# Kernel tuning notes

Measured on AMD Instinct MI355X. Metric: run time of the kernel, lower is better.

The kernel has to match this reference:

```python
import jax, jax.numpy as jnp
import numpy as np

KS = 3      # kernel_size
PAD = 1     # padding
GROUPS = 4

def _patches(a, H, W):
    # a: [B, C, H+2*PAD, W+2*PAD] -> [B, C, H, W, KS, KS]
    return jnp.stack([
        jnp.stack([a[:, :, i:i + H, j:j + W] for j in range(KS)], axis=-1)
        for i in range(KS)], axis=-2)

def setup_inputs() -> dict:
    key = jax.random.key(0)
    ks = jax.random.split(key, 7)
    B, Cin, Cout, H, W = 8, 256, 256, 64, 64
    std = np.sqrt(2.0 / Cout)  # kaiming fan_out
    return {
        "x": jax.random.normal(ks[0], (B, Cin, H, W), jnp.float32),
        "y": jax.random.normal(ks[1], (B, Cin, H, W), jnp.float32),
        "wq": jax.random.normal(ks[2], (Cout, Cin), jnp.float32) * std,
        "wk": jax.random.normal(ks[3], (Cout, Cin), jnp.float32) * std,
        "wv": jax.random.normal(ks[4], (Cout, Cin), jnp.float32) * std,
        "rel_h": jax.random.normal(ks[5], (Cout // 2, 1, 1, KS, 1), jnp.float32),
        "rel_w": jax.random.normal(ks[6], (Cout // 2, 1, 1, 1, KS), jnp.float32),
    }

def reference(x, y, wq, wk, wv, rel_h, rel_w):
    B, _, H, W = x.shape
    Cout = wq.shape[0]
    half = Cout // 2
    xp = jnp.pad(x, ((0, 0), (0, 0), (PAD, PAD), (PAD, PAD)))
    q = jnp.einsum('oi,bihw->bohw', wq, y)          # [B,Cout,H,W]
    k = jnp.einsum('oi,bihw->bohw', wk, xp)         # [B,Cout,H+2,W+2]
    v = jnp.einsum('oi,bihw->bohw', wv, xp)
    kp = _patches(k, H, W)                          # [B,Cout,H,W,KS,KS]
    vp = _patches(v, H, W)
    kp = jnp.concatenate([kp[:, :half] + rel_h[None], kp[:, half:] + rel_w[None]], axis=1)
    cg = Cout // GROUPS
    kp = kp.reshape(B, GROUPS, cg, H, W, KS * KS)
    vp = vp.reshape(B, GROUPS, cg, H, W, KS * KS)
    qg = q.reshape(B, GROUPS, cg, H, W, 1)
    attn = jax.nn.softmax(qg * kp, axis=-1)         # per-channel softmax over window
    out = jnp.einsum('bnchwk,bnchwk->bnchw', attn, vp)
    return out.reshape(B, Cout, H, W)
```

## Files before the change

### kernel.cpp

```cpp
#include <hip/hip_runtime.h>
#include <hip/hip_bf16.h>
#include <stdint.h>

typedef __attribute__((ext_vector_type(8))) short short8;
typedef __attribute__((ext_vector_type(4))) float floatx4;
typedef __attribute__((ext_vector_type(4))) unsigned int uintx4;
typedef __attribute__((ext_vector_type(2))) unsigned int uintx2;
typedef unsigned int u32;

#define HH 64
#define WW 64
#define HWSZ 4096
#define BB 8
#define CIN 256
#define COUT 256
#define NTOT 32768

#define GLL16(g, l)                                                            \
    __builtin_amdgcn_global_load_lds(                                          \
        (const __attribute__((address_space(1))) u32*)(const void*)(g),        \
        (__attribute__((address_space(3))) u32*)(void*)(l), 16, 0, 0)

__device__ __forceinline__ unsigned short f2b(float f) {
    union { float f; unsigned int u; } v; v.f = f;
    unsigned int r = v.u + 0x7FFFu + ((v.u >> 16) & 1u);
    return (unsigned short)(r >> 16);
}
__device__ __forceinline__ float b2f(unsigned short h) {
    union { unsigned int u; float f; } v; v.u = ((unsigned int)h) << 16;
    return v.f;
}

__global__ __launch_bounds__(256) void transpose_cast(
        const float* __restrict__ y, const float* __restrict__ x,
        unsigned short* __restrict__ yT, unsigned short* __restrict__ xT) {
    __shared__ float lt[64 * 65];
    int zz = blockIdx.z;
    int which = zz & 1;
    int b = zz >> 1;
    const float* src = which ? x : y;
    unsigned short* dst = which ? xT : yT;
    int p0 = blockIdx.x * 64;
    int c0 = blockIdx.y * 64;
    int t = threadIdx.x;

    const float* sp = src + ((size_t)b * CIN + c0) * HWSZ + p0;
    int chL = t >> 4;
    int pxL = (t & 15) * 4;
    #pragma unroll
    for (int pass = 0; pass < 4; ++pass) {
        int ch = chL + pass * 16;
        float4 v = *(const float4*)(sp + (size_t)ch * HWSZ + pxL);
        lt[ch * 65 + pxL + 0] = v.x;
        lt[ch * 65 + pxL + 1] = v.y;
        lt[ch * 65 + pxL + 2] = v.z;
        lt[ch * 65 + pxL + 3] = v.w;
    }
    __syncthreads();

    int c8 = (t & 7) * 8;
    int pxR = t >> 3;
    unsigned short* dp = dst + ((size_t)b * HWSZ + p0) * CIN + c0 + c8;
    #pragma unroll
    for (int pass = 0; pass < 2; ++pass) {
        int px = pxR + pass * 32;
        unsigned int dw[4];
        #pragma unroll
        for (int j = 0; j < 4; ++j) {
            float lo = lt[(c8 + 2 * j) * 65 + px];
            float hi = lt[(c8 + 2 * j + 1) * 65 + px];
            dw[j] = (unsigned int)f2b(lo) | ((unsigned int)f2b(hi) << 16);
        }
        *(uintx4*)(dp + (size_t)px * CIN) = (uintx4){dw[0], dw[1], dw[2], dw[3]};
    }
}

__global__ void wcast(const float* __restrict__ wq, const float* __restrict__ wk,
                      const float* __restrict__ wv,
                      unsigned short* __restrict__ wqb, unsigned short* __restrict__ wkb,
                      unsigned short* __restrict__ wvb) {
    int idx = blockIdx.x * 256 + threadIdx.x;
    wqb[idx] = f2b(wq[idx]);
    wkb[idx] = f2b(wk[idx]);
    wvb[idx] = f2b(wv[idx]);
}

__global__ __launch_bounds__(256)
void gemm_qkv(const unsigned short* __restrict__ wqb, const unsigned short* __restrict__ wkb,
              const unsigned short* __restrict__ wvb,
              const unsigned short* __restrict__ yT, const unsigned short* __restrict__ xT,
              unsigned short* __restrict__ Qb, unsigned short* __restrict__ Kb,
              unsigned short* __restrict__ Vb) {
    __shared__ unsigned short lA[2][128 * 32];
    __shared__ unsigned short lB[2][128 * 32];

    int z = blockIdx.z;
    const unsigned short* Wb = (z == 0) ? wqb : (z == 1) ? wkb : wvb;
    const unsigned short* In = (z == 0) ? yT : xT;
    unsigned short* Out = (z == 0) ? Qb : (z == 1) ? Kb : Vb;

    int n0 = blockIdx.x * 128;
    int m0 = blockIdx.y * 128;
    int t = threadIdx.x;
    int lane = t & 63;
    int wave = t >> 6;
    int quad = lane >> 4;
    int l16 = lane & 15;
    int wm = (wave >> 1) * 64;
    int wn = (wave & 1) * 64;

    int sA0 = t >> 2;
    int cch = (t & 3) * 8;
    int sB0 = t >> 2;
    int sB1 = 64 + (t >> 2);
    int gnB0 = 4 * (sB0 & 31) + (sB0 >> 5);
    int gnB1 = 4 * (sB1 & 31) + (sB1 >> 5);

    const unsigned short* gA0 = Wb + (size_t)(m0 + sA0) * CIN + cch;
    const unsigned short* gA1 = Wb + (size_t)(m0 + sA0 + 64) * CIN + cch;
    const unsigned short* gB0 = In + (size_t)(n0 + gnB0) * CIN + cch;
    const unsigned short* gB1 = In + (size_t)(n0 + gnB1) * CIN + cch;

    floatx4 acc[4][4];
    #pragma unroll
    for (int mi = 0; mi < 4; ++mi)
        #pragma unroll
        for (int ni = 0; ni < 4; ++ni)
            acc[mi][ni] = (floatx4){0.f, 0.f, 0.f, 0.f};

    #pragma unroll
    for (int it = 0; it < 4; ++it) {
        int k0 = it * 64;
        #pragma unroll
        for (int bsel = 0; bsel < 2; ++bsel) {
            int ko = k0 + bsel * 32;
            unsigned short* dA = lA[bsel] + wave * 512;
            unsigned short* dB = lB[bsel] + wave * 512;
            GLL16(gA0 + ko, dA);
            GLL16(gA1 + ko, dA + 2048);
            GLL16(gB0 + ko, dB);
            GLL16(gB1 + ko, dB + 2048);
        }
        __syncthreads();

        #pragma unroll
        for (int bsel = 0; bsel < 2; ++bsel) {
            short8 af[4], bf[4];
            #pragma unroll
            for (int mi = 0; mi < 4; ++mi)
                af[mi] = *(const short8*)(lA[bsel] + (wm + mi * 16 + l16) * 32 + quad * 8);
            #pragma unroll
            for (int ni = 0; ni < 4; ++ni)
                bf[ni] = *(const short8*)(lB[bsel] + (ni * 32 + (wn >> 2) + l16) * 32 + quad * 8);
            #pragma unroll
            for (int mi = 0; mi < 4; ++mi)
                #pragma unroll
                for (int ni = 0; ni < 4; ++ni)
                    acc[mi][ni] = __builtin_amdgcn_mfma_f32_16x16x32_bf16(af[mi], bf[ni], acc[mi][ni], 0, 0, 0);
        }
        __syncthreads();
    }

    int colb = n0 + wn + 4 * l16;
    #pragma unroll
    for (int mi = 0; mi < 4; ++mi) {
        #pragma unroll
        for (int r = 0; r < 4; ++r) {
            int row = m0 + wm + mi * 16 + quad * 4 + r;
            unsigned int lo = (unsigned int)f2b(acc[mi][0][r]) | ((unsigned int)f2b(acc[mi][1][r]) << 16);
            unsigned int hi = (unsigned int)f2b(acc[mi][2][r]) | ((unsigned int)f2b(acc[mi][3][r]) << 16);
            *(uintx2*)(Out + (size_t)row * NTOT + colb) = (uintx2){lo, hi};
        }
    }
}

__global__ __launch_bounds__(256)
void attn(const unsigned short* __restrict__ Q,
          const unsigned short* __restrict__ K,
          const unsigned short* __restrict__ V,
          const float* __restrict__ rel_h,
          const float* __restrict__ rel_w,
          float* __restrict__ out) {
    int gid = blockIdx.x * 256 + threadIdx.x;
    int w8 = gid & 7;
    int w0 = w8 << 3;
    int h = (gid >> 3) & 63;
    int c = (gid >> 9) & 255;
    int b = gid >> 17;

    size_t nb = (size_t)c * NTOT + (size_t)b * HWSZ;
    const unsigned short* Kp = K + nb;
    const unsigned short* Vp = V + nb;

    short8 qr = *(const short8*)(Q + nb + h * 64 + w0);

    bool use_h = (c < 128);
    float rel3[3];
    if (use_h) {
        rel3[0] = rel_h[c * 3 + 0]; rel3[1] = rel_h[c * 3 + 1]; rel3[2] = rel_h[c * 3 + 2];
    } else {
        int cc = c - 128;
        rel3[0] = rel_w[cc * 3 + 0]; rel3[1] = rel_w[cc * 3 + 1]; rel3[2] = rel_w[cc * 3 + 2];
    }
    float rr[9];
    #pragma unroll
    for (int r = 0; r < 3; ++r)
        #pragma unroll
        for (int j = 0; j < 3; ++j)
            rr[r * 3 + j] = use_h ? rel3[r] : rel3[j];

    int e0 = (w0 > 0) ? w0 - 1 : 0;
    int e9 = (w0 < 56) ? w0 + 8 : 63;
    bool okL = (w0 > 0);
    bool okR = (w0 < 56);

    float kb[3][10], vb[3][10];
    #pragma unroll
    for (int r = 0; r < 3; ++r) {
        int ihr = h + r - 1;
        bool rok = (unsigned)ihr < 64u;
        int ihc = ihr < 0 ? 0 : (ihr > 63 ? 63 : ihr);
        int ro = ihc * 64;
        short8 km = *(const short8*)(Kp + ro + w0);
        short8 vm = *(const short8*)(Vp + ro + w0);
        float ke0 = b2f(Kp[ro + e0]), ve0 = b2f(Vp[ro + e0]);
        float ke9 = b2f(Kp[ro + e9]), ve9 = b2f(Vp[ro + e9]);
        #pragma unroll
        for (int i = 0; i < 8; ++i) {
            kb[r][i + 1] = rok ? b2f((unsigned short)km[i]) : 0.f;
            vb[r][i + 1] = rok ? b2f((unsigned short)vm[i]) : 0.f;
        }
        bool ok0 = rok && okL;
        bool ok9 = rok && okR;
        kb[r][0] = ok0 ? ke0 : 0.f;  vb[r][0] = ok0 ? ve0 : 0.f;
        kb[r][9] = ok9 ? ke9 : 0.f;  vb[r][9] = ok9 ? ve9 : 0.f;
    }

    float q[8];
    #pragma unroll
    for (int i = 0; i < 8; ++i) q[i] = b2f((unsigned short)qr[i]);

    float ov[8];
    #pragma unroll
    for (int wi = 0; wi < 8; ++wi) {
        float qv = q[wi];
        float lg[9];
        #pragma unroll
        for (int r = 0; r < 3; ++r)
            #pragma unroll
            for (int j = 0; j < 3; ++j)
                lg[r * 3 + j] = qv * (kb[r][wi + j] + rr[r * 3 + j]);
        float m = lg[0];
        #pragma unroll
        for (int t2 = 1; t2 < 9; ++t2) m = fmaxf(m, lg[t2]);
        float s = 0.f, o = 0.f;
        #pragma unroll
        for (int r = 0; r < 3; ++r)
            #pragma unroll
            for (int j = 0; j < 3; ++j) {
                float e = __expf(lg[r * 3 + j] - m);
                s += e;
                o += e * vb[r][wi + j];
            }
        ov[wi] = o * __builtin_amdgcn_rcpf(s);
    }

    size_t oi = ((size_t)b * COUT + c) * HWSZ + h * 64 + w0;
    *(floatx4*)(out + oi)     = (floatx4){ ov[0], ov[1], ov[2], ov[3] };
    *(floatx4*)(out + oi + 4) = (floatx4){ ov[4], ov[5], ov[6], ov[7] };
}

extern "C" void kernel_launch(void* const* d_in, const int* in_sizes, int n_in,
                              void* d_out, int out_size, void* d_ws, size_t ws_size,
                              hipStream_t stream) {
    const float* x = (const float*)d_in[0];
    const float* y = (const float*)d_in[1];
    const float* wq = (const float*)d_in[2];
    const float* wk = (const float*)d_in[3];
    const float* wv = (const float*)d_in[4];
    const float* rel_h = (const float*)d_in[5];
    const float* rel_w = (const float*)d_in[6];
    float* out = (float*)d_out;

    char* ws = (char*)d_ws;
    unsigned short* yT  = (unsigned short*)(ws);
    unsigned short* xT  = (unsigned short*)(ws + 16777216);
    unsigned short* wqb = (unsigned short*)(ws + 33554432);
    unsigned short* wkb = (unsigned short*)(ws + 33554432 + 131072);
    unsigned short* wvb = (unsigned short*)(ws + 33554432 + 262144);
    unsigned short* Qb  = (unsigned short*)(ws + 33947648);
    unsigned short* Kb  = (unsigned short*)(ws + 33947648 + 16777216);
    unsigned short* Vb  = (unsigned short*)(ws + 33947648 + 33554432);

    transpose_cast<<<dim3(64, 4, 16), 256, 0, stream>>>(y, x, yT, xT);
    wcast<<<256, 256, 0, stream>>>(wq, wk, wv, wqb, wkb, wvb);
    gemm_qkv<<<dim3(256, 2, 3), 256, 0, stream>>>(wqb, wkb, wvb, yT, xT, Qb, Kb, Vb);
    attn<<<4096, 256, 0, stream>>>(Qb, Kb, Vb, rel_h, rel_w, out);
}
```

Before: 158.9 us.

## Fuse input transpose and bf16 cast into QKV GEMM B-tile loads

Drops the separate transpose_cast kernel. The GEMM now reads fp32 x/y directly in NCHW layout, converts to bf16 with v_cvt_pk_bf16_f32, and writes the B tile to LDS in a swizzled layout. Next-iteration B loads are prefetched into registers to overlap with MFMA work. This removes a full read/write round trip of the activations and one launch. In exchange, each of the m-blocks and the K and V passes now re-read the fp32 input (more global traffic than the bf16 copy) and register pressure rises.

```diff
diff --git a/kernel.cpp b/kernel.cpp
--- a/kernel.cpp
+++ b/kernel.cpp
@@ -30,49 +30,10 @@
     union { unsigned int u; float f; } v; v.u = ((unsigned int)h) << 16;
     return v.f;
 }
-
-__global__ __launch_bounds__(256) void transpose_cast(
-        const float* __restrict__ y, const float* __restrict__ x,
-        unsigned short* __restrict__ yT, unsigned short* __restrict__ xT) {
-    __shared__ float lt[64 * 65];
-    int zz = blockIdx.z;
-    int which = zz & 1;
-    int b = zz >> 1;
-    const float* src = which ? x : y;
-    unsigned short* dst = which ? xT : yT;
-    int p0 = blockIdx.x * 64;
-    int c0 = blockIdx.y * 64;
-    int t = threadIdx.x;
-
-    const float* sp = src + ((size_t)b * CIN + c0) * HWSZ + p0;
-    int chL = t >> 4;
-    int pxL = (t & 15) * 4;
-    #pragma unroll
-    for (int pass = 0; pass < 4; ++pass) {
-        int ch = chL + pass * 16;
-        float4 v = *(const float4*)(sp + (size_t)ch * HWSZ + pxL);
-        lt[ch * 65 + pxL + 0] = v.x;
-        lt[ch * 65 + pxL + 1] = v.y;
-        lt[ch * 65 + pxL + 2] = v.z;
-        lt[ch * 65 + pxL + 3] = v.w;
-    }
-    __syncthreads();
-
-    int c8 = (t & 7) * 8;
-    int pxR = t >> 3;
-    unsigned short* dp = dst + ((size_t)b * HWSZ + p0) * CIN + c0 + c8;
-    #pragma unroll
-    for (int pass = 0; pass < 2; ++pass) {
-        int px = pxR + pass * 32;
-        unsigned int dw[4];
-        #pragma unroll
-        for (int j = 0; j < 4; ++j) {
-            float lo = lt[(c8 + 2 * j) * 65 + px];
-            float hi = lt[(c8 + 2 * j + 1) * 65 + px];
-            dw[j] = (unsigned int)f2b(lo) | ((unsigned int)f2b(hi) << 16);
-        }
-        *(uintx4*)(dp + (size_t)px * CIN) = (uintx4){dw[0], dw[1], dw[2], dw[3]};
-    }
+__device__ __forceinline__ unsigned int pk2(float lo, float hi) {
+    unsigned int r;
+    asm("v_cvt_pk_bf16_f32 %0, %1, %2" : "=v"(r) : "v"(lo), "v"(hi));
+    return r;
 }
 
 __global__ void wcast(const float* __restrict__ wq, const float* __restrict__ wk,
@@ -88,7 +49,7 @@
 __global__ __launch_bounds__(256)
 void gemm_qkv(const unsigned short* __restrict__ wqb, const unsigned short* __restrict__ wkb,
               const unsigned short* __restrict__ wvb,
-              const unsigned short* __restrict__ yT, const unsigned short* __restrict__ xT,
+              const float* __restrict__ xf, const float* __restrict__ yf,
               unsigned short* __restrict__ Qb, unsigned short* __restrict__ Kb,
               unsigned short* __restrict__ Vb) {
     __shared__ unsigned short lA[2][128 * 32];
@@ -96,11 +57,13 @@
 
     int z = blockIdx.z;
     const unsigned short* Wb = (z == 0) ? wqb : (z == 1) ? wkb : wvb;
-    const unsigned short* In = (z == 0) ? yT : xT;
+    const float* In = (z == 0) ? yf : xf;
     unsigned short* Out = (z == 0) ? Qb : (z == 1) ? Kb : Vb;
 
     int n0 = blockIdx.x * 128;
     int m0 = blockIdx.y * 128;
+    int b  = n0 >> 12;
+    int p0 = n0 & 4095;
     int t = threadIdx.x;
     int lane = t & 63;
     int wave = t >> 6;
@@ -111,15 +74,23 @@
 
     int sA0 = t >> 2;
     int cch = (t & 3) * 8;
-    int sB0 = t >> 2;
-    int sB1 = 64 + (t >> 2);
-    int gnB0 = 4 * (sB0 & 31) + (sB0 >> 5);
-    int gnB1 = 4 * (sB1 & 31) + (sB1 >> 5);
-
     const unsigned short* gA0 = Wb + (size_t)(m0 + sA0) * CIN + cch;
     const unsigned short* gA1 = Wb + (size_t)(m0 + sA0 + 64) * CIN + cch;
-    const unsigned short* gB0 = In + (size_t)(n0 + gnB0) * CIN + cch;
-    const unsigned short* gB1 = In + (size_t)(n0 + gnB1) * CIN + cch;
+
+    int ng = (t & 31) * 4;
+    int kq = (t >> 5) * 4;
+    const float* gB = In + ((size_t)b * CIN + kq) * HWSZ + p0 + ng;
+    int sbase = t & 31;
+    int wr_idx[4];
+    #pragma unroll
+    for (int j = 0; j < 4; ++j) {
+        int s = j * 32 + sbase;
+        wr_idx[j] = s * 32 + (((kq >> 3) ^ ((s >> 1) & 3)) << 3) + (kq & 4);
+    }
+
+    int rB = (wn >> 2) + l16;
+    int swzr = (rB >> 1) & 3;
+    int rd_off = rB * 32 + ((quad ^ swzr) << 3);
 
     floatx4 acc[4][4];
     #pragma unroll
@@ -128,30 +99,51 @@
         for (int ni = 0; ni < 4; ++ni)
             acc[mi][ni] = (floatx4){0.f, 0.f, 0.f, 0.f};
 
+    floatx4 pb[2][4];
+    #pragma unroll
+    for (int bs = 0; bs < 2; ++bs)
+        #pragma unroll
+        for (int i = 0; i < 4; ++i)
+            pb[bs][i] = *(const floatx4*)(gB + (size_t)(bs * 32 + i) * HWSZ);
+
     #pragma unroll
     for (int it = 0; it < 4; ++it) {
         int k0 = it * 64;
         #pragma unroll
-        for (int bsel = 0; bsel < 2; ++bsel) {
-            int ko = k0 + bsel * 32;
-            unsigned short* dA = lA[bsel] + wave * 512;
-            unsigned short* dB = lB[bsel] + wave * 512;
+        for (int bs = 0; bs < 2; ++bs) {
+            int ko = k0 + bs * 32;
+            unsigned short* dA = lA[bs] + wave * 512;
             GLL16(gA0 + ko, dA);
             GLL16(gA1 + ko, dA + 2048);
-            GLL16(gB0 + ko, dB);
-            GLL16(gB1 + ko, dB + 2048);
+        }
+        floatx4 nb[2][4];
+        if (it < 3) {
+            #pragma unroll
+            for (int bs = 0; bs < 2; ++bs)
+                #pragma unroll
+                for (int i = 0; i < 4; ++i)
+                    nb[bs][i] = *(const floatx4*)(gB + (size_t)(k0 + 64 + bs * 32 + i) * HWSZ);
+        }
+        #pragma unroll
+        for (int bs = 0; bs < 2; ++bs) {
+            #pragma unroll
+            for (int j = 0; j < 4; ++j) {
+                unsigned int d0 = pk2(pb[bs][0][j], pb[bs][1][j]);
+                unsigned int d1 = pk2(pb[bs][2][j], pb[bs][3][j]);
+                *(uintx2*)(lB[bs] + wr_idx[j]) = (uintx2){d0, d1};
+            }
         }
         __syncthreads();
 
         #pragma unroll
-        for (int bsel = 0; bsel < 2; ++bsel) {
+        for (int bs = 0; bs < 2; ++bs) {
             short8 af[4], bf[4];
             #pragma unroll
             for (int mi = 0; mi < 4; ++mi)
-                af[mi] = *(const short8*)(lA[bsel] + (wm + mi * 16 + l16) * 32 + quad * 8);
+                af[mi] = *(const short8*)(lA[bs] + (wm + mi * 16 + l16) * 32 + quad * 8);
             #pragma unroll
             for (int ni = 0; ni < 4; ++ni)
-                bf[ni] = *(const short8*)(lB[bsel] + (ni * 32 + (wn >> 2) + l16) * 32 + quad * 8);
+                bf[ni] = *(const short8*)(lB[bs] + rd_off + ni * 1024);
             #pragma unroll
             for (int mi = 0; mi < 4; ++mi)
                 #pragma unroll
@@ -159,6 +151,14 @@
                     acc[mi][ni] = __builtin_amdgcn_mfma_f32_16x16x32_bf16(af[mi], bf[ni], acc[mi][ni], 0, 0, 0);
         }
         __syncthreads();
+
+        if (it < 3) {
+            #pragma unroll
+            for (int bs = 0; bs < 2; ++bs)
+                #pragma unroll
+                for (int i = 0; i < 4; ++i)
+                    pb[bs][i] = nb[bs][i];
+        }
     }
 
     int colb = n0 + wn + 4 * l16;
@@ -283,8 +283,6 @@
     float* out = (float*)d_out;
 
     char* ws = (char*)d_ws;
-    unsigned short* yT  = (unsigned short*)(ws);
-    unsigned short* xT  = (unsigned short*)(ws + 16777216);
     unsigned short* wqb = (unsigned short*)(ws + 33554432);
     unsigned short* wkb = (unsigned short*)(ws + 33554432 + 131072);
     unsigned short* wvb = (unsigned short*)(ws + 33554432 + 262144);
@@ -292,8 +290,7 @@
     unsigned short* Kb  = (unsigned short*)(ws + 33947648 + 16777216);
     unsigned short* Vb  = (unsigned short*)(ws + 33947648 + 33554432);
 
-    transpose_cast<<<dim3(64, 4, 16), 256, 0, stream>>>(y, x, yT, xT);
     wcast<<<256, 256, 0, stream>>>(wq, wk, wv, wqb, wkb, wvb);
-    gemm_qkv<<<dim3(256, 2, 3), 256, 0, stream>>>(wqb, wkb, wvb, yT, xT, Qb, Kb, Vb);
+    gemm_qkv<<<dim3(256, 2, 3), 256, 0, stream>>>(wqb, wkb, wvb, x, y, Qb, Kb, Vb);
     attn<<<4096, 256, 0, stream>>>(Qb, Kb, Vb, rel_h, rel_w, out);
 }
```

After: 152.2 us. 4.3% less time.
